# Kernel tuning notes

Hardware: AMD Instinct MI355X
Metric: run time of the kernel (lower is better)

The kernel has to match this reference:

```python
import jax, jax.numpy as jnp
import numpy as np

B, H, W, C = 8, 256, 256, 64   # n_heads == d_model == C (forced by q.reshape), n_groups == 1
KER, PAD = 5, 2
SCALE = C ** -0.5              # module uses scale_factor = d_model**-0.5


def conv1x1(x, w, b):
    # x [B,C,H,W], w [O,C] (1x1 conv == per-pixel matmul)
    return jnp.einsum('bchw,oc->bohw', x, w) + b[None, :, None, None]


def grid_sample_bilinear(img, grid):
    # img [B,C,H,W]; grid [B,H,W,2] = (x,y) normalized coords; align_corners=False, zeros padding
    Bb, Cc, Hh, Ww = img.shape
    gx, gy = grid[..., 0], grid[..., 1]
    ix = ((gx + 1.0) * Ww - 1.0) * 0.5
    iy = ((gy + 1.0) * Hh - 1.0) * 0.5
    ix0, iy0 = jnp.floor(ix), jnp.floor(iy)
    wx1, wy1 = ix - ix0, iy - iy0
    wx0, wy0 = 1.0 - wx1, 1.0 - wy1
    imf = img.reshape(Bb, Cc, Hh * Ww)

    def gather(xi, yi):
        valid = (xi >= 0) & (xi < Ww) & (yi >= 0) & (yi < Hh)
        xi_c = jnp.clip(xi, 0, Ww - 1).astype(jnp.int32)
        yi_c = jnp.clip(yi, 0, Hh - 1).astype(jnp.int32)
        idx = jnp.broadcast_to((yi_c * Ww + xi_c).reshape(Bb, 1, Hh * Ww), (Bb, Cc, Hh * Ww))
        v = jnp.take_along_axis(imf, idx, axis=2).reshape(Bb, Cc, Hh, Ww)
        return v * valid[:, None, :, :].astype(img.dtype)

    return (gather(ix0, iy0) * (wx0 * wy0)[:, None]
            + gather(ix0 + 1.0, iy0) * (wx1 * wy0)[:, None]
            + gather(ix0, iy0 + 1.0) * (wx0 * wy1)[:, None]
            + gather(ix0 + 1.0, iy0 + 1.0) * (wx1 * wy1)[:, None])


def setup_inputs():
    key = jax.random.key(0)
    ks = jax.random.split(key, 12)
    s = 0.05
    return {
        'x': jax.random.normal(ks[0], (B, H, W, C), jnp.float32),
        'Wq': jax.random.normal(ks[1], (C, C), jnp.float32) * s,
        'bq': jnp.zeros((C,), jnp.float32),
        'Wk': jax.random.normal(ks[2], (C, C), jnp.float32) * s,
        'bk': jnp.zeros((C,), jnp.float32),
        'Wv': jax.random.normal(ks[3], (C, C), jnp.float32) * s,
        'bv': jnp.zeros((C,), jnp.float32),
        'Woff1': jax.random.normal(ks[4], (C, C, KER, KER), jnp.float32) * 0.02,
        'boff1': jnp.zeros((C,), jnp.float32),
        'Woff2': jax.random.normal(ks[5], (2, C), jnp.float32) * 0.02,
        'rpb': jax.random.normal(ks[6], (1, C, H, 1), jnp.float32) * 0.02,
        'Wout': jax.random.normal(ks[7], (C, C), jnp.float32) * s,
        'bout': jnp.zeros((C,), jnp.float32),
    }


def reference(x, Wq, bq, Wk, bk, Wv, bv, Woff1, boff1, Woff2, rpb, Wout, bout):
    xc = jnp.transpose(x, (0, 3, 1, 2))                          # [B,C,H,W]
    q = conv1x1(xc, Wq, bq)
    # offset head: 5x5 conv (same padding) -> 1x1 conv to 2 channels (no bias)
    o = jax.lax.conv_general_dilated(q, Woff1, (1, 1), [(PAD, PAD), (PAD, PAD)],
                                     dimension_numbers=('NCHW', 'OIHW', 'NCHW'))
    o = o + boff1[None, :, None, None]
    offset = jnp.tanh(jnp.einsum('bchw,oc->bohw', o, Woff2)) * KER   # [B,2,H,W]
    # grid: channel 0 = x coords, channel 1 = y coords (torch meshgrid indexing='xy')
    xx, yy = jnp.meshgrid(jnp.arange(W, dtype=x.dtype), jnp.arange(H, dtype=x.dtype), indexing='xy')
    vg = jnp.stack([xx, yy], 0)[None] + offset                   # [B,2,H,W]
    # faithful to source normalize_grid: x-channel divided by (H-1), y-channel by (W-1)
    gxn = 2.0 * vg[:, 0] / max(H - 1, 1) - 1.0
    gyn = 2.0 * vg[:, 1] / max(W - 1, 1) - 1.0
    grid_s = jnp.stack([gxn, gyn], -1)                           # [B,H,W,2]
    x_sampled = grid_sample_bilinear(xc, grid_s)                 # [B,C,H,W]
    k = conv1x1(x_sampled, Wk, bk)
    v = conv1x1(x_sampled, Wv, bv) + rpb                         # rpb [1,C,H,1] broadcasts (seq_len==H)
    qf = q.reshape(B * C, H, W)                                  # n_heads == C
    kf = k.reshape(B * C, H, W)
    vf = v.reshape(B * C, H, W)
    scores = jnp.einsum('bid,bjd->bij', qf, kf) * SCALE          # attend over H, feature dim = W
    attn = jax.nn.softmax(scores, axis=-1)
    out = jnp.einsum('bij,bjd->bid', attn, vf).reshape(B, H, W, C)  # raw reshape, as in source
    return jnp.einsum('bhwc,oc->bhwo', out, Wout) + bout
```

## Files before the change

### kernel.cpp

```cpp
#include <hip/hip_runtime.h>
#include <math.h>

#define NPIX 524288

typedef __attribute__((ext_vector_type(8))) short short8b;
typedef __attribute__((ext_vector_type(4))) float f32x4;
#define MFMA16 __builtin_amdgcn_mfma_f32_16x16x32_bf16

__device__ inline unsigned short bf16_rn(float x) {
    unsigned u = __float_as_uint(x);
    unsigned r = (u + 0x7FFFu + ((u >> 16) & 1u)) >> 16;
    return (unsigned short)r;
}
__device__ inline float bf16_f(unsigned short h) {
    return __uint_as_float(((unsigned)h) << 16);
}
__device__ inline void tsplit1(float a, unsigned short& h, unsigned short& l) {
    unsigned u = __float_as_uint(a);
    h = (unsigned short)(u >> 16);
    float r = a - __uint_as_float(u & 0xFFFF0000u);
    l = (unsigned short)(__float_as_uint(r) >> 16);
}
__device__ inline void tsplit4(float a, float b, float c, float d, ushort4& hv, ushort4& lv) {
    tsplit1(a, hv.x, lv.x);
    tsplit1(b, hv.y, lv.y);
    tsplit1(c, hv.z, lv.z);
    tsplit1(d, hv.w, lv.w);
}

__global__ void build_wcomb_kernel(const float* __restrict__ Woff1,
                                   const float* __restrict__ boff1,
                                   const float* __restrict__ Woff2,
                                   float* __restrict__ wcomb,
                                   float* __restrict__ bcomb) {
    int idx = blockIdx.x * 256 + threadIdx.x;
    if (idx < 2 * 64 * 25) {
        int p = idx / 1600;
        int rest = idx - p * 1600;
        float s = 0.f;
        for (int cm = 0; cm < 64; ++cm)
            s += Woff2[p * 64 + cm] * Woff1[cm * 1600 + rest];
        wcomb[idx] = s;
    }
    if (idx < 2) {
        float s = 0.f;
        for (int cm = 0; cm < 64; ++cm) s += Woff2[idx * 64 + cm] * boff1[cm];
        bcomb[idx] = s;
    }
}

__global__ void build_wcat_kernel(const float* __restrict__ Wq, const float* __restrict__ bq,
                                  const float* __restrict__ wcomb,
                                  unsigned short* __restrict__ wcath,
                                  unsigned short* __restrict__ wcatl,
                                  float* __restrict__ bcat) {
    int idx = blockIdx.x * 256 + threadIdx.x;
    if (idx < 8192) {
        int r = idx >> 6, c = idx & 63;
        float v = 0.f;
        if (r < 64) v = Wq[r * 64 + c] * 0.125f;
        else if (r < 114) {
            int ch = r - 64, p = ch / 25, tap = ch % 25;
            for (int cin = 0; cin < 64; ++cin)
                v += wcomb[p * 1600 + cin * 25 + tap] * Wq[cin * 64 + c];
        }
        unsigned short hh = bf16_rn(v);
        wcath[idx] = hh;
        wcatl[idx] = bf16_rn(v - bf16_f(hh));
    }
    if (idx >= 8192 && idx < 8192 + 128) {
        int r = idx - 8192;
        float v = 0.f;
        if (r < 64) v = bq[r] * 0.125f;
        else if (r < 114) {
            int ch = r - 64, p = ch / 25, tap = ch % 25;
            for (int cin = 0; cin < 64; ++cin)
                v += wcomb[p * 1600 + cin * 25 + tap] * bq[cin];
        }
        bcat[r] = v;
    }
}

__global__ void build_wfixed_kernel(const float* __restrict__ Wk, const float* __restrict__ Wv,
                                    const float* __restrict__ Wout,
                                    unsigned short* __restrict__ wkvh, unsigned short* __restrict__ wkvl,
                                    unsigned short* __restrict__ wouth, unsigned short* __restrict__ woutl) {
    int idx = blockIdx.x * 256 + threadIdx.x;
    if (idx < 8192) {
        float v = (idx < 4096) ? Wk[idx] : Wv[idx - 4096];
        unsigned short hh = bf16_rn(v);
        wkvh[idx] = hh;
        wkvl[idx] = bf16_rn(v - bf16_f(hh));
    } else if (idx < 12288) {
        float v = Wout[idx - 8192];
        unsigned short hh = bf16_rn(v);
        wouth[idx - 8192] = hh;
        woutl[idx - 8192] = bf16_rn(v - bf16_f(hh));
    }
}

__global__ __launch_bounds__(256)
void convqp_kernel(const float* __restrict__ in, const unsigned short* __restrict__ wh,
                   const unsigned short* __restrict__ wl, const float* __restrict__ bcat,
                   unsigned short* __restrict__ qh, float* __restrict__ projout) {
    __shared__ unsigned short a_hi[64 * 72], a_lo[64 * 72];
    int t = threadIdx.x;
    int p = t & 63, w = t >> 6;
    int pix0 = blockIdx.x * 64;
    {
        const float4* src = (const float4*)(in + (size_t)(pix0 + p) * 64 + w * 16);
#pragma unroll
        for (int u4 = 0; u4 < 4; ++u4) {
            float4 v = src[u4];
            ushort4 hv, lv;
            tsplit4(v.x, v.y, v.z, v.w, hv, lv);
            *(ushort4*)&a_hi[p * 72 + w * 16 + u4 * 4] = hv;
            *(ushort4*)&a_lo[p * 72 + w * 16 + u4 * 4] = lv;
        }
    }
    __syncthreads();
    int lrow = t & 15, lgrp = (t & 63) >> 4;
    int wc = w * 32;
    f32x4 acc[4][2];
#pragma unroll
    for (int mi = 0; mi < 4; ++mi)
#pragma unroll
        for (int nj = 0; nj < 2; ++nj) acc[mi][nj] = (f32x4){0.f, 0.f, 0.f, 0.f};
#pragma unroll
    for (int dk = 0; dk < 2; ++dk) {
        int k0 = dk * 32 + lgrp * 8;
        short8b bh[2], bl[2];
#pragma unroll
        for (int nj = 0; nj < 2; ++nj) {
            int c = wc + nj * 16 + lrow;
            bh[nj] = *(const short8b*)(wh + c * 64 + k0);
            bl[nj] = *(const short8b*)(wl + c * 64 + k0);
        }
#pragma unroll
        for (int mi = 0; mi < 4; ++mi) {
            int r = mi * 16 + lrow;
            short8b ah = *(short8b*)&a_hi[r * 72 + k0];
            short8b al = *(short8b*)&a_lo[r * 72 + k0];
#pragma unroll
            for (int nj = 0; nj < 2; ++nj) {
                acc[mi][nj] = MFMA16(ah, bh[nj], acc[mi][nj], 0, 0, 0);
                acc[mi][nj] = MFMA16(ah, bl[nj], acc[mi][nj], 0, 0, 0);
                acc[mi][nj] = MFMA16(al, bh[nj], acc[mi][nj], 0, 0, 0);
            }
        }
    }
    int b = pix0 >> 16, hw0 = pix0 & 65535;
#pragma unroll
    for (int nj = 0; nj < 2; ++nj) {
        int c = wc + nj * 16 + lrow;
        if (c < 64) {
            float bias = bcat[c];
            size_t o = (((size_t)(b * 64 + c)) << 16) + hw0;
#pragma unroll
            for (int mi = 0; mi < 4; ++mi) {
                ushort4 hv;
                hv.x = bf16_rn(acc[mi][nj][0] + bias);
                hv.y = bf16_rn(acc[mi][nj][1] + bias);
                hv.z = bf16_rn(acc[mi][nj][2] + bias);
                hv.w = bf16_rn(acc[mi][nj][3] + bias);
                *(ushort4*)(qh + o + mi * 16 + lgrp * 4) = hv;
            }
        } else if (c < 114) {
            float bias = bcat[c];
            float* dst = projout + (((size_t)(b * 50 + (c - 64))) << 16) + hw0;
#pragma unroll
            for (int mi = 0; mi < 4; ++mi) {
                float4 o;
                o.x = acc[mi][nj][0] + bias;
                o.y = acc[mi][nj][1] + bias;
                o.z = acc[mi][nj][2] + bias;
                o.w = acc[mi][nj][3] + bias;
                *(float4*)(dst + mi * 16 + lgrp * 4) = o;
            }
        }
    }
}

__global__ __launch_bounds__(256)
void offset_gather_kernel(const float* __restrict__ proj, const float* __restrict__ bcomb,
                          float2* __restrict__ coords) {
    int x = threadIdx.x, y = blockIdx.x, b = blockIdx.y;
    const float* pb = proj + (((size_t)b * 50) << 16);
    float a0 = bcomb[0], a1 = bcomb[1];
#pragma unroll
    for (int ky = 0; ky < 5; ++ky) {
        int yy = y + ky - 2;
        if (yy < 0 || yy >= 256) continue;
#pragma unroll
        for (int kx = 0; kx < 5; ++kx) {
            int xx = x + kx - 2;
            if (xx < 0 || xx >= 256) continue;
            int tap = ky * 5 + kx;
            size_t off = (size_t)yy * 256 + xx;
            a0 += pb[((size_t)tap << 16) + off];
            a1 += pb[((size_t)(25 + tap) << 16) + off];
        }
    }
    float ox = tanhf(a0) * 5.f, oy = tanhf(a1) * 5.f;
    float vgx = (float)x + ox, vgy = (float)y + oy;
    float ix = vgx * (256.f / 255.f) - 0.5f;
    float iy = vgy * (256.f / 255.f) - 0.5f;
    coords[(((size_t)b) << 16) + y * 256 + x] = make_float2(ix, iy);
}

__global__ __launch_bounds__(256)
void sample_kv_kernel(const float* __restrict__ x, const float2* __restrict__ coords,
                      const unsigned short* __restrict__ wh, const unsigned short* __restrict__ wl,
                      const float* __restrict__ bk, const float* __restrict__ bv,
                      const float* __restrict__ rpb,
                      unsigned short* __restrict__ khi, unsigned short* __restrict__ vthi) {
    __shared__ char smem[18432 + 2048];
    unsigned short* a_hi = (unsigned short*)smem;
    unsigned short* a_lo = (unsigned short*)(smem + 9216);
    unsigned short* stg  = (unsigned short*)smem;
    float* rpbl = (float*)(smem + 18432);

    int t = threadIdx.x;
    int b = blockIdx.x >> 10, pidx = blockIdx.x & 1023;
    int h0 = (pidx >> 5) * 8, w0 = (pidx & 31) * 8;
    int w = t >> 6;
    {
        int i0 = t * 2;
        rpbl[i0]     = rpb[(i0 >> 3) * 256 + h0 + (i0 & 7)];
        rpbl[i0 + 1] = rpb[((i0 + 1) >> 3) * 256 + h0 + ((i0 + 1) & 7)];
    }
    {
        int pg = t >> 2, wg = t & 3;
        int dyg = pg >> 3, dxg = pg & 7;
        int hwg = (h0 + dyg) * 256 + (w0 + dxg);
        float2 cc = coords[(((size_t)b) << 16) + hwg];
        float ix0f = floorf(cc.x), iy0f = floorf(cc.y);
        float wx1 = cc.x - ix0f, wy1 = cc.y - iy0f;
        float wx0 = 1.f - wx1, wy0 = 1.f - wy1;
        int ix0 = (int)ix0f, iy0 = (int)iy0f;
        float s[16];
#pragma unroll
        for (int u = 0; u < 16; ++u) s[u] = 0.f;
        const float* xb = x + (((size_t)b) << 16) * 64 + wg * 16;
        int cxs[4] = {ix0, ix0 + 1, ix0, ix0 + 1};
        int cys[4] = {iy0, iy0, iy0 + 1, iy0 + 1};
        float ws4[4] = {wx0 * wy0, wx1 * wy0, wx0 * wy1, wx1 * wy1};
#pragma unroll
        for (int cr = 0; cr < 4; ++cr) {
            int cx = cxs[cr], cy = cys[cr];
            if (cx >= 0 && cx < 256 && cy >= 0 && cy < 256) {
                float wgt = ws4[cr];
                const float4* sp = (const float4*)(xb + ((size_t)(cy * 256 + cx) << 6));
#pragma unroll
                for (int q4 = 0; q4 < 4; ++q4) {
                    float4 v = sp[q4];
                    s[4 * q4] += wgt * v.x; s[4 * q4 + 1] += wgt * v.y;
                    s[4 * q4 + 2] += wgt * v.z; s[4 * q4 + 3] += wgt * v.w;
                }
            }
        }
#pragma unroll
        for (int u4 = 0; u4 < 4; ++u4) {
            ushort4 hv, lv;
            tsplit4(s[u4 * 4], s[u4 * 4 + 1], s[u4 * 4 + 2], s[u4 * 4 + 3], hv, lv);
            *(ushort4*)&a_hi[pg * 72 + wg * 16 + u4 * 4] = hv;
            *(ushort4*)&a_lo[pg * 72 + wg * 16 + u4 * 4] = lv;
        }
    }
    __syncthreads();
    int lrow = t & 15, lgrp = (t & 63) >> 4;
    int wc = w * 32;
    f32x4 acc[4][2];
#pragma unroll
    for (int mi = 0; mi < 4; ++mi)
#pragma unroll
        for (int nj = 0; nj < 2; ++nj) acc[mi][nj] = (f32x4){0.f, 0.f, 0.f, 0.f};
#pragma unroll
    for (int dk = 0; dk < 2; ++dk) {
        int k0 = dk * 32 + lgrp * 8;
        short8b bh[2], bl[2];
#pragma unroll
        for (int nj = 0; nj < 2; ++nj) {
            int c = wc + nj * 16 + lrow;
            bh[nj] = *(const short8b*)(wh + c * 64 + k0);
            bl[nj] = *(const short8b*)(wl + c * 64 + k0);
        }
#pragma unroll
        for (int mi = 0; mi < 4; ++mi) {
            int r = mi * 16 + lrow;
            short8b ah = *(short8b*)&a_hi[r * 72 + k0];
            short8b al = *(short8b*)&a_lo[r * 72 + k0];
#pragma unroll
            for (int nj = 0; nj < 2; ++nj) {
                acc[mi][nj] = MFMA16(ah, bh[nj], acc[mi][nj], 0, 0, 0);
                acc[mi][nj] = MFMA16(ah, bl[nj], acc[mi][nj], 0, 0, 0);
                acc[mi][nj] = MFMA16(al, bh[nj], acc[mi][nj], 0, 0, 0);
            }
        }
    }
    __syncthreads();
#pragma unroll
    for (int nj = 0; nj < 2; ++nj) {
        int c = wc + nj * 16 + lrow;
        if (c < 64) {
            float bias = bk[c];
#pragma unroll
            for (int mi = 0; mi < 4; ++mi) {
                int p0 = mi * 16 + lgrp * 4;
                ushort4 hv;
                hv.x = bf16_rn(acc[mi][nj][0] + bias);
                hv.y = bf16_rn(acc[mi][nj][1] + bias);
                hv.z = bf16_rn(acc[mi][nj][2] + bias);
                hv.w = bf16_rn(acc[mi][nj][3] + bias);
                *(ushort4*)&stg[c * 72 + p0] = hv;
            }
        } else {
            int cv = c - 64;
#pragma unroll
            for (int mi = 0; mi < 4; ++mi) {
                int dyg = mi * 2 + (lgrp >> 1);
                float bias = bv[cv] + rpbl[cv * 8 + dyg];
                int dxb = (lgrp & 1) * 4;
#pragma unroll
                for (int rr = 0; rr < 4; ++rr) {
                    float vv = acc[mi][nj][rr] + bias;
                    stg[4608 + cv * 72 + (dxb + rr) * 8 + dyg] = bf16_rn(vv);
                }
            }
        }
    }
    __syncthreads();
    {
        int pl = t >> 7, c = (t >> 1) & 63, half = t & 1;
        const unsigned short* src = &stg[pl * 4608 + c * 72 + half * 32];
        unsigned short* dstp = pl ? vthi : khi;
        size_t hb = ((size_t)(b * 64 + c)) << 16;
        size_t tb = pl ? (size_t)((w0 >> 3) * 2048 + (h0 >> 3) * 64)
                       : (size_t)((h0 >> 3) * 2048 + (w0 >> 3) * 64);
        unsigned short* dst = dstp + hb + tb + half * 32;
#pragma unroll
        for (int r2 = 0; r2 < 4; ++r2)
            *(short8b*)(dst + r2 * 8) = *(const short8b*)(src + r2 * 8);
    }
}

__global__ __launch_bounds__(512, 4)
void attn_mfma_kernel(unsigned short* __restrict__ qh, unsigned short* __restrict__ ql,
                      const unsigned short* __restrict__ khig,
                      const unsigned short* __restrict__ vthig) {
    __shared__ char sm[68608];
    unsigned short* qs = (unsigned short*)sm;
    unsigned short* ps = (unsigned short*)sm;
    float* ost = (float*)sm;
    float* reds = (float*)(sm + 66560);

    int t = threadIdx.x;
    int lane = t & 63, w = t >> 6;
    int lrow = lane & 15, lgrp = lane >> 4;
    int wc = w * 32;

    int bid = blockIdx.x;
    int xcd = bid & 7, r = bid >> 3;
    int head = xcd * 64 + (r >> 2), rt = r & 3;
    size_t qfb = ((size_t)head << 16) + (size_t)rt * 64 * 256;
    const unsigned short* kh = khig + ((size_t)head << 16);
    const unsigned short* vth = vthig + ((size_t)head << 16);

    {
        int row = t >> 3, cb = (t & 7) * 32;
        const unsigned short* s0 = qh + qfb + row * 256 + cb;
        unsigned short* d0 = &qs[row * 264 + cb];
#pragma unroll
        for (int u = 0; u < 4; ++u)
            *(short8b*)(d0 + u * 8) = *(const short8b*)(s0 + u * 8);
    }
    __syncthreads();

    int j0r = wc + lrow, j1r = wc + 16 + lrow;
    size_t jo0 = (size_t)((j0r >> 3) * 2048 + (j0r & 7) * 8);
    size_t jo1 = (size_t)((j1r >> 3) * 2048 + (j1r & 7) * 8);

    f32x4 acc[4][2];
#pragma unroll
    for (int mi = 0; mi < 4; ++mi)
#pragma unroll
        for (int nj = 0; nj < 2; ++nj) acc[mi][nj] = (f32x4){0.f, 0.f, 0.f, 0.f};

#pragma unroll
    for (int s = 0; s < 8; ++s) {
        int k0 = s * 32 + lgrp * 8;
        size_t doff = (size_t)((s * 4 + lgrp) * 64);
        short8b bh0 = *(const short8b*)(kh + jo0 + doff);
        short8b bh1 = *(const short8b*)(kh + jo1 + doff);
#pragma unroll
        for (int mi = 0; mi < 4; ++mi) {
            short8b ah = *(short8b*)&qs[(mi * 16 + lrow) * 264 + k0];
            acc[mi][0] = MFMA16(ah, bh0, acc[mi][0], 0, 0, 0);
            acc[mi][1] = MFMA16(ah, bh1, acc[mi][1], 0, 0, 0);
        }
    }
    __syncthreads();

#pragma unroll
    for (int mi = 0; mi < 4; ++mi)
#pragma unroll
        for (int rr = 0; rr < 4; ++rr) {
            int row = mi * 16 + lgrp * 4 + rr;
            float p0 = __expf(acc[mi][0][rr]);
            float p1 = __expf(acc[mi][1][rr]);
            ps[row * 264 + wc + lrow] = bf16_rn(p0);
            ps[row * 264 + wc + 16 + lrow] = bf16_rn(p1);
            float ls = p0 + p1;
            ls += __shfl_xor(ls, 1);
            ls += __shfl_xor(ls, 2);
            ls += __shfl_xor(ls, 4);
            ls += __shfl_xor(ls, 8);
            if (lrow == 0) reds[w * 64 + row] = ls;
        }
    __syncthreads();

#pragma unroll
    for (int mi = 0; mi < 4; ++mi)
#pragma unroll
        for (int nd = 0; nd < 2; ++nd) acc[mi][nd] = (f32x4){0.f, 0.f, 0.f, 0.f};

#pragma unroll
    for (int jc = 0; jc < 8; ++jc) {
        int j0 = jc * 32 + lgrp * 8;
        size_t joff = (size_t)((jc * 4 + lgrp) * 64);
        short8b vh0 = *(const short8b*)(vth + jo0 + joff);
        short8b vh1 = *(const short8b*)(vth + jo1 + joff);
#pragma unroll
        for (int mi = 0; mi < 4; ++mi) {
            short8b pa = *(short8b*)&ps[(mi * 16 + lrow) * 264 + j0];
            acc[mi][0] = MFMA16(pa, vh0, acc[mi][0], 0, 0, 0);
            acc[mi][1] = MFMA16(pa, vh1, acc[mi][1], 0, 0, 0);
        }
    }
    __syncthreads();

    float invl[4][4];
#pragma unroll
    for (int mi = 0; mi < 4; ++mi)
#pragma unroll
        for (int rr = 0; rr < 4; ++rr) {
            int row = mi * 16 + lgrp * 4 + rr;
            float l = 0.f;
#pragma unroll
            for (int ww = 0; ww < 8; ++ww) l += reds[ww * 64 + row];
            invl[mi][rr] = 1.f / l;
        }
#pragma unroll
    for (int mi = 0; mi < 4; ++mi)
#pragma unroll
        for (int nd = 0; nd < 2; ++nd)
#pragma unroll
            for (int rr = 0; rr < 4; ++rr)
                ost[(mi * 16 + lgrp * 4 + rr) * 260 + wc + nd * 16 + lrow] =
                    acc[mi][nd][rr] * invl[mi][rr];
    __syncthreads();
#pragma unroll
    for (int it = 0; it < 8; ++it) {
        int id = it * 512 + t;
        int row = id >> 6, col4 = (id & 63) * 4;
        float4 vv = *(float4*)&ost[row * 260 + col4];
        ushort4 hv, lv;
        tsplit4(vv.x, vv.y, vv.z, vv.w, hv, lv);
        *(ushort4*)(qh + qfb + row * 256 + col4) = hv;
        *(ushort4*)(ql + qfb + row * 256 + col4) = lv;
    }
}

__global__ __launch_bounds__(256)
void convout_kernel(const unsigned short* __restrict__ oh, const unsigned short* __restrict__ ol,
                    const unsigned short* __restrict__ wh, const unsigned short* __restrict__ wl,
                    const float* __restrict__ bias, float* __restrict__ out) {
    __shared__ unsigned short a_hi[64 * 72], a_lo[64 * 72];
    int t = threadIdx.x;
    int p = t & 63, w = t >> 6;
    size_t pix0 = (size_t)blockIdx.x * 64;
    {
        const unsigned short* s0 = oh + (pix0 + p) * 64 + w * 16;
        const unsigned short* s1 = ol + (pix0 + p) * 64 + w * 16;
        *(short8b*)&a_hi[p * 72 + w * 16]     = *(const short8b*)(s0);
        *(short8b*)&a_hi[p * 72 + w * 16 + 8] = *(const short8b*)(s0 + 8);
        *(short8b*)&a_lo[p * 72 + w * 16]     = *(const short8b*)(s1);
        *(short8b*)&a_lo[p * 72 + w * 16 + 8] = *(const short8b*)(s1 + 8);
    }
    __syncthreads();
    int lrow = t & 15, lgrp = (t & 63) >> 4;
    int c = w * 16 + lrow;
    f32x4 acc[4];
#pragma unroll
    for (int mi = 0; mi < 4; ++mi) acc[mi] = (f32x4){0.f, 0.f, 0.f, 0.f};
#pragma unroll
    for (int dk = 0; dk < 2; ++dk) {
        int k0 = dk * 32 + lgrp * 8;
        short8b bh = *(const short8b*)(wh + c * 64 + k0);
        short8b bl = *(const short8b*)(wl + c * 64 + k0);
#pragma unroll
        for (int mi = 0; mi < 4; ++mi) {
            int r = mi * 16 + lrow;
            short8b ah = *(short8b*)&a_hi[r * 72 + k0];
            short8b al = *(short8b*)&a_lo[r * 72 + k0];
            acc[mi] = MFMA16(ah, bh, acc[mi], 0, 0, 0);
            acc[mi] = MFMA16(ah, bl, acc[mi], 0, 0, 0);
            acc[mi] = MFMA16(al, bh, acc[mi], 0, 0, 0);
        }
    }
    float bb = bias[c];
#pragma unroll
    for (int mi = 0; mi < 4; ++mi) {
        size_t px0 = pix0 + mi * 16 + lgrp * 4;
#pragma unroll
        for (int rr = 0; rr < 4; ++rr)
            out[(px0 + rr) * 64 + c] = acc[mi][rr] + bb;
    }
}

extern "C" void kernel_launch(void* const* d_in, const int* in_sizes, int n_in,
                              void* d_out, int out_size, void* d_ws, size_t ws_size,
                              hipStream_t stream) {
    const float* x     = (const float*)d_in[0];
    const float* Wq    = (const float*)d_in[1];
    const float* bq    = (const float*)d_in[2];
    const float* Wk    = (const float*)d_in[3];
    const float* bk    = (const float*)d_in[4];
    const float* Wv    = (const float*)d_in[5];
    const float* bv    = (const float*)d_in[6];
    const float* Woff1 = (const float*)d_in[7];
    const float* boff1 = (const float*)d_in[8];
    const float* Woff2 = (const float*)d_in[9];
    const float* rpb   = (const float*)d_in[10];
    const float* Wout  = (const float*)d_in[11];
    const float* bout  = (const float*)d_in[12];
    float* out = (float*)d_out;

    char* wsb = (char*)d_ws;
    unsigned short* qh  = (unsigned short*)wsb;
    unsigned short* ql  = qh + (size_t)NPIX * 64;
    unsigned short* khi = ql + (size_t)NPIX * 64;
    unsigned short* klo = khi + (size_t)NPIX * 64;
    unsigned short* vthi = klo + (size_t)NPIX * 64;
    unsigned short* vtlo = vthi + (size_t)NPIX * 64;
    float* coords = (float*)(vtlo + (size_t)NPIX * 64);
    float* wcomb  = coords + (size_t)NPIX * 2;
    float* bcomb  = wcomb + 3200;
    float* bcat   = bcomb + 2;
    unsigned short* wcath = (unsigned short*)(bcat + 128);
    unsigned short* wcatl = wcath + 8192;
    unsigned short* wkvh  = wcatl + 8192;
    unsigned short* wkvl  = wkvh + 8192;
    unsigned short* wouth = wkvl + 8192;
    unsigned short* woutl = wouth + 4096;
    float* proj = (float*)khi;

    build_wcomb_kernel<<<13, 256, 0, stream>>>(Woff1, boff1, Woff2, wcomb, bcomb);
    build_wcat_kernel<<<33, 256, 0, stream>>>(Wq, bq, wcomb, wcath, wcatl, bcat);
    build_wfixed_kernel<<<48, 256, 0, stream>>>(Wk, Wv, Wout, wkvh, wkvl, wouth, woutl);
    convqp_kernel<<<NPIX / 64, 256, 0, stream>>>(x, wcath, wcatl, bcat, qh, proj);
    offset_gather_kernel<<<dim3(256, 8), 256, 0, stream>>>(proj, bcomb, (float2*)coords);
    sample_kv_kernel<<<NPIX / 64, 256, 0, stream>>>(x, (const float2*)coords, wkvh, wkvl,
                                                    bk, bv, rpb, khi, vthi);
    attn_mfma_kernel<<<2048, 512, 0, stream>>>(qh, ql, khi, vthi);
    convout_kernel<<<NPIX / 64, 256, 0, stream>>>(qh, ql, wouth, woutl, bout, out);
}
```

Before: 394.3 us.

## Drop activation low-part split and store offset projections in bf16

Activations fed to MFMA are now rounded to a single bf16 instead of hi/lo split, so each GEMM does two MFMAs per tile instead of three and the lo LDS buffers and ql output are removed. The 50-channel offset projection is stored as bf16 rather than fp32, halving that intermediate's write and read traffic. Weight splits now use truncation for the hi part. This reduces compute, memory traffic and shared memory at the cost of reduced precision, especially in the sampling offsets.

```diff
diff --git a/kernel.cpp b/kernel.cpp
--- a/kernel.cpp
+++ b/kernel.cpp
@@ -20,12 +20,6 @@
     h = (unsigned short)(u >> 16);
     float r = a - __uint_as_float(u & 0xFFFF0000u);
     l = (unsigned short)(__float_as_uint(r) >> 16);
-}
-__device__ inline void tsplit4(float a, float b, float c, float d, ushort4& hv, ushort4& lv) {
-    tsplit1(a, hv.x, lv.x);
-    tsplit1(b, hv.y, lv.y);
-    tsplit1(c, hv.z, lv.z);
-    tsplit1(d, hv.w, lv.w);
 }
 
 __global__ void build_wcomb_kernel(const float* __restrict__ Woff1,
@@ -64,9 +58,10 @@
             for (int cin = 0; cin < 64; ++cin)
                 v += wcomb[p * 1600 + cin * 25 + tap] * Wq[cin * 64 + c];
         }
-        unsigned short hh = bf16_rn(v);
+        unsigned short hh, ll;
+        tsplit1(v, hh, ll);
         wcath[idx] = hh;
-        wcatl[idx] = bf16_rn(v - bf16_f(hh));
+        wcatl[idx] = ll;
     }
     if (idx >= 8192 && idx < 8192 + 128) {
         int r = idx - 8192;
@@ -88,22 +83,24 @@
     int idx = blockIdx.x * 256 + threadIdx.x;
     if (idx < 8192) {
         float v = (idx < 4096) ? Wk[idx] : Wv[idx - 4096];
-        unsigned short hh = bf16_rn(v);
+        unsigned short hh, ll;
+        tsplit1(v, hh, ll);
         wkvh[idx] = hh;
-        wkvl[idx] = bf16_rn(v - bf16_f(hh));
+        wkvl[idx] = ll;
     } else if (idx < 12288) {
         float v = Wout[idx - 8192];
-        unsigned short hh = bf16_rn(v);
+        unsigned short hh, ll;
+        tsplit1(v, hh, ll);
         wouth[idx - 8192] = hh;
-        woutl[idx - 8192] = bf16_rn(v - bf16_f(hh));
+        woutl[idx - 8192] = ll;
     }
 }
 
 __global__ __launch_bounds__(256)
 void convqp_kernel(const float* __restrict__ in, const unsigned short* __restrict__ wh,
                    const unsigned short* __restrict__ wl, const float* __restrict__ bcat,
-                   unsigned short* __restrict__ qh, float* __restrict__ projout) {
-    __shared__ unsigned short a_hi[64 * 72], a_lo[64 * 72];
+                   unsigned short* __restrict__ qh, unsigned short* __restrict__ projout) {
+    __shared__ unsigned short a_s[64 * 72];
     int t = threadIdx.x;
     int p = t & 63, w = t >> 6;
     int pix0 = blockIdx.x * 64;
@@ -112,10 +109,10 @@
 #pragma unroll
         for (int u4 = 0; u4 < 4; ++u4) {
             float4 v = src[u4];
-            ushort4 hv, lv;
-            tsplit4(v.x, v.y, v.z, v.w, hv, lv);
-            *(ushort4*)&a_hi[p * 72 + w * 16 + u4 * 4] = hv;
-            *(ushort4*)&a_lo[p * 72 + w * 16 + u4 * 4] = lv;
+            ushort4 hv;
+            hv.x = bf16_rn(v.x); hv.y = bf16_rn(v.y);
+            hv.z = bf16_rn(v.z); hv.w = bf16_rn(v.w);
+            *(ushort4*)&a_s[p * 72 + w * 16 + u4 * 4] = hv;
         }
     }
     __syncthreads();
@@ -139,13 +136,11 @@
 #pragma unroll
         for (int mi = 0; mi < 4; ++mi) {
             int r = mi * 16 + lrow;
-            short8b ah = *(short8b*)&a_hi[r * 72 + k0];
-            short8b al = *(short8b*)&a_lo[r * 72 + k0];
+            short8b ah = *(short8b*)&a_s[r * 72 + k0];
 #pragma unroll
             for (int nj = 0; nj < 2; ++nj) {
                 acc[mi][nj] = MFMA16(ah, bh[nj], acc[mi][nj], 0, 0, 0);
                 acc[mi][nj] = MFMA16(ah, bl[nj], acc[mi][nj], 0, 0, 0);
-                acc[mi][nj] = MFMA16(al, bh[nj], acc[mi][nj], 0, 0, 0);
             }
         }
     }
@@ -167,25 +162,25 @@
             }
         } else if (c < 114) {
             float bias = bcat[c];
-            float* dst = projout + (((size_t)(b * 50 + (c - 64))) << 16) + hw0;
+            unsigned short* dst = projout + (((size_t)(b * 50 + (c - 64))) << 16) + hw0;
 #pragma unroll
             for (int mi = 0; mi < 4; ++mi) {
-                float4 o;
-                o.x = acc[mi][nj][0] + bias;
-                o.y = acc[mi][nj][1] + bias;
-                o.z = acc[mi][nj][2] + bias;
-                o.w = acc[mi][nj][3] + bias;
-                *(float4*)(dst + mi * 16 + lgrp * 4) = o;
+                ushort4 hv;
+                hv.x = bf16_rn(acc[mi][nj][0] + bias);
+                hv.y = bf16_rn(acc[mi][nj][1] + bias);
+                hv.z = bf16_rn(acc[mi][nj][2] + bias);
+                hv.w = bf16_rn(acc[mi][nj][3] + bias);
+                *(ushort4*)(dst + mi * 16 + lgrp * 4) = hv;
             }
         }
     }
 }
 
 __global__ __launch_bounds__(256)
-void offset_gather_kernel(const float* __restrict__ proj, const float* __restrict__ bcomb,
+void offset_gather_kernel(const unsigned short* __restrict__ proj, const float* __restrict__ bcomb,
                           float2* __restrict__ coords) {
     int x = threadIdx.x, y = blockIdx.x, b = blockIdx.y;
-    const float* pb = proj + (((size_t)b * 50) << 16);
+    const unsigned short* pb = proj + (((size_t)b * 50) << 16);
     float a0 = bcomb[0], a1 = bcomb[1];
 #pragma unroll
     for (int ky = 0; ky < 5; ++ky) {
@@ -197,8 +192,8 @@
             if (xx < 0 || xx >= 256) continue;
             int tap = ky * 5 + kx;
             size_t off = (size_t)yy * 256 + xx;
-            a0 += pb[((size_t)tap << 16) + off];
-            a1 += pb[((size_t)(25 + tap) << 16) + off];
+            a0 += bf16_f(pb[((size_t)tap << 16) + off]);
+            a1 += bf16_f(pb[((size_t)(25 + tap) << 16) + off]);
         }
     }
     float ox = tanhf(a0) * 5.f, oy = tanhf(a1) * 5.f;
@@ -215,9 +210,8 @@
                       const float* __restrict__ rpb,
                       unsigned short* __restrict__ khi, unsigned short* __restrict__ vthi) {
     __shared__ char smem[18432 + 2048];
-    unsigned short* a_hi = (unsigned short*)smem;
-    unsigned short* a_lo = (unsigned short*)(smem + 9216);
-    unsigned short* stg  = (unsigned short*)smem;
+    unsigned short* a_s = (unsigned short*)smem;
+    unsigned short* stg = (unsigned short*)smem;
     float* rpbl = (float*)(smem + 18432);
 
     int t = threadIdx.x;
@@ -261,10 +255,10 @@
         }
 #pragma unroll
         for (int u4 = 0; u4 < 4; ++u4) {
-            ushort4 hv, lv;
-            tsplit4(s[u4 * 4], s[u4 * 4 + 1], s[u4 * 4 + 2], s[u4 * 4 + 3], hv, lv);
-            *(ushort4*)&a_hi[pg * 72 + wg * 16 + u4 * 4] = hv;
-            *(ushort4*)&a_lo[pg * 72 + wg * 16 + u4 * 4] = lv;
+            ushort4 hv;
+            hv.x = bf16_rn(s[u4 * 4]);     hv.y = bf16_rn(s[u4 * 4 + 1]);
+            hv.z = bf16_rn(s[u4 * 4 + 2]); hv.w = bf16_rn(s[u4 * 4 + 3]);
+            *(ushort4*)&a_s[pg * 72 + wg * 16 + u4 * 4] = hv;
         }
     }
     __syncthreads();
@@ -288,13 +282,11 @@
 #pragma unroll
         for (int mi = 0; mi < 4; ++mi) {
             int r = mi * 16 + lrow;
-            short8b ah = *(short8b*)&a_hi[r * 72 + k0];
-            short8b al = *(short8b*)&a_lo[r * 72 + k0];
+            short8b ah = *(short8b*)&a_s[r * 72 + k0];
 #pragma unroll
             for (int nj = 0; nj < 2; ++nj) {
                 acc[mi][nj] = MFMA16(ah, bh[nj], acc[mi][nj], 0, 0, 0);
                 acc[mi][nj] = MFMA16(ah, bl[nj], acc[mi][nj], 0, 0, 0);
-                acc[mi][nj] = MFMA16(al, bh[nj], acc[mi][nj], 0, 0, 0);
             }
         }
     }
@@ -345,7 +337,7 @@
 }
 
 __global__ __launch_bounds__(512, 4)
-void attn_mfma_kernel(unsigned short* __restrict__ qh, unsigned short* __restrict__ ql,
+void attn_mfma_kernel(unsigned short* __restrict__ qh,
                       const unsigned short* __restrict__ khig,
                       const unsigned short* __restrict__ vthig) {
     __shared__ char sm[68608];
@@ -464,28 +456,25 @@
         int id = it * 512 + t;
         int row = id >> 6, col4 = (id & 63) * 4;
         float4 vv = *(float4*)&ost[row * 260 + col4];
-        ushort4 hv, lv;
-        tsplit4(vv.x, vv.y, vv.z, vv.w, hv, lv);
+        ushort4 hv;
+        hv.x = bf16_rn(vv.x); hv.y = bf16_rn(vv.y);
+        hv.z = bf16_rn(vv.z); hv.w = bf16_rn(vv.w);
         *(ushort4*)(qh + qfb + row * 256 + col4) = hv;
-        *(ushort4*)(ql + qfb + row * 256 + col4) = lv;
     }
 }
 
 __global__ __launch_bounds__(256)
-void convout_kernel(const unsigned short* __restrict__ oh, const unsigned short* __restrict__ ol,
+void convout_kernel(const unsigned short* __restrict__ oh,
                     const unsigned short* __restrict__ wh, const unsigned short* __restrict__ wl,
                     const float* __restrict__ bias, float* __restrict__ out) {
-    __shared__ unsigned short a_hi[64 * 72], a_lo[64 * 72];
+    __shared__ unsigned short a_s[64 * 72];
     int t = threadIdx.x;
     int p = t & 63, w = t >> 6;
     size_t pix0 = (size_t)blockIdx.x * 64;
     {
         const unsigned short* s0 = oh + (pix0 + p) * 64 + w * 16;
-        const unsigned short* s1 = ol + (pix0 + p) * 64 + w * 16;
-        *(short8b*)&a_hi[p * 72 + w * 16]     = *(const short8b*)(s0);
-        *(short8b*)&a_hi[p * 72 + w * 16 + 8] = *(const short8b*)(s0 + 8);
-        *(short8b*)&a_lo[p * 72 + w * 16]     = *(const short8b*)(s1);
-        *(short8b*)&a_lo[p * 72 + w * 16 + 8] = *(const short8b*)(s1 + 8);
+        *(short8b*)&a_s[p * 72 + w * 16]     = *(const short8b*)(s0);
+        *(short8b*)&a_s[p * 72 + w * 16 + 8] = *(const short8b*)(s0 + 8);
     }
     __syncthreads();
     int lrow = t & 15, lgrp = (t & 63) >> 4;
@@ -501,11 +490,9 @@
 #pragma unroll
         for (int mi = 0; mi < 4; ++mi) {
             int r = mi * 16 + lrow;
-            short8b ah = *(short8b*)&a_hi[r * 72 + k0];
-            short8b al = *(short8b*)&a_lo[r * 72 + k0];
+            short8b ah = *(short8b*)&a_s[r * 72 + k0];
             acc[mi] = MFMA16(ah, bh, acc[mi], 0, 0, 0);
             acc[mi] = MFMA16(ah, bl, acc[mi], 0, 0, 0);
-            acc[mi] = MFMA16(al, bh, acc[mi], 0, 0, 0);
         }
     }
     float bb = bias[c];
@@ -553,7 +540,7 @@
     unsigned short* wkvl  = wkvh + 8192;
     unsigned short* wouth = wkvl + 8192;
     unsigned short* woutl = wouth + 4096;
-    float* proj = (float*)khi;
+    unsigned short* proj = ql;
 
     build_wcomb_kernel<<<13, 256, 0, stream>>>(Woff1, boff1, Woff2, wcomb, bcomb);
     build_wcat_kernel<<<33, 256, 0, stream>>>(Wq, bq, wcomb, wcath, wcatl, bcat);
@@ -562,6 +549,6 @@
     offset_gather_kernel<<<dim3(256, 8), 256, 0, stream>>>(proj, bcomb, (float2*)coords);
     sample_kv_kernel<<<NPIX / 64, 256, 0, stream>>>(x, (const float2*)coords, wkvh, wkvl,
                                                     bk, bv, rpb, khi, vthi);
-    attn_mfma_kernel<<<2048, 512, 0, stream>>>(qh, ql, khi, vthi);
-    convout_kernel<<<NPIX / 64, 256, 0, stream>>>(qh, ql, wouth, woutl, bout, out);
-}
+    attn_mfma_kernel<<<2048, 512, 0, stream>>>(qh, khi, vthi);
+    convout_kernel<<<NPIX / 64, 256, 0, stream>>>(qh, wouth, woutl, bout, out);
+}
```

Result: faster. 340.3 us (-13.7%).
